# Kernel tuning notes

Measured on AMD Instinct MI355X. Metric: run time of the kernel, lower is better.

The kernel has to match this reference:

```python
import jax, jax.numpy as jnp
import numpy as np

LN_EPS = 1e-5


def setup_inputs() -> dict:
    key = jax.random.key(0)
    ks = jax.random.split(key, 6)
    N_NODES, N_EDGES, D, H, E = 100000, 20000, 128, 64, 1000000
    node_feat = jax.random.normal(ks[0], (N_NODES, D), dtype=jnp.float32)
    edge_feat = jax.random.normal(ks[1], (N_EDGES, D), dtype=jnp.float32)
    gamma = jnp.ones((2 * D,), dtype=jnp.float32)
    beta = jnp.zeros((2 * D,), dtype=jnp.float32)
    # xavier_uniform-like init
    lim1 = float(np.sqrt(6.0 / (2 * D + H)))
    lim2 = float(np.sqrt(6.0 / (H + 1)))
    W1 = jax.random.uniform(ks[2], (2 * D, H), minval=-lim1, maxval=lim1, dtype=jnp.float32)
    b1 = jnp.zeros((H,), dtype=jnp.float32)
    W2 = jax.random.uniform(ks[3], (H, 1), minval=-lim2, maxval=lim2, dtype=jnp.float32)
    b2 = jnp.zeros((1,), dtype=jnp.float32)
    node_idx = jax.random.randint(ks[4], (E,), 0, N_NODES, dtype=jnp.int64 if jax.config.read('jax_enable_x64') else jnp.int32)
    edge_idx = jax.random.randint(ks[5], (E,), 0, N_EDGES, dtype=node_idx.dtype)
    return {"node_feat": node_feat, "edge_feat": edge_feat, "gamma": gamma, "beta": beta,
            "W1": W1, "b1": b1, "W2": W2, "b2": b2,
            "node_idx": node_idx, "edge_idx": edge_idx}


def reference(node_feat, edge_feat, gamma, beta, W1, b1, W2, b2, node_idx, edge_idx):
    # Gather incidence-pair embeddings: [E, D] each
    emb_node = node_feat[node_idx]
    emb_edge = edge_feat[edge_idx]
    # combined: [E, 2D], order = [edge, node] as in torch.cat([emb_edge, emb_node], 1)
    combined = jnp.concatenate([emb_edge, emb_node], axis=1)
    # LayerNorm over last dim
    mu = jnp.mean(combined, axis=-1, keepdims=True)
    var = jnp.var(combined, axis=-1, keepdims=True)
    xn = (combined - mu) * jax.lax.rsqrt(var + LN_EPS) * gamma + beta
    # MLP: Linear -> ReLU -> Linear, output [E, 1]
    h = jax.nn.relu(xn @ W1 + b1)
    return h @ W2 + b2
```

## Files before the change

kernel.cpp:

```cpp
#include <hip/hip_runtime.h>

#define LN_EPS 1e-5f
#define DD 128
#define TWO_D 256
#define HH 64

typedef unsigned int uint;
typedef __attribute__((ext_vector_type(8))) short short8v;
typedef __attribute__((ext_vector_type(4))) float f32x4;

__device__ __forceinline__ unsigned short f2bf(float f) {
    uint u = __float_as_uint(f);
    u += 0x7FFFu + ((u >> 16) & 1u);
    return (unsigned short)(u >> 16);
}
__device__ __forceinline__ float bf2f(unsigned short h) {
    return __uint_as_float(((uint)h) << 16);
}

__global__ __launch_bounds__(256) void k_fused(
    const float* __restrict__ node_feat, int n_nodes, int nbN,
    const float* __restrict__ edge_feat, int n_edges,
    const float* __restrict__ gamma, const float* __restrict__ beta,
    const float* __restrict__ W1, const float* __restrict__ b1,
    signed char* __restrict__ node_pt, float4* __restrict__ node_st,
    signed char* __restrict__ edge_pt, float4* __restrict__ edge_st,
    float* __restrict__ GB) {
    int bid = blockIdx.x;
    int tid = threadIdx.x;

    if (bid == 0) {
        if (tid < 128) {
            int h = tid & 63;
            bool isB = tid >= 64;
            float acc = isB ? b1[h] : 0.f;
            const float* coef = isB ? beta : gamma;
#pragma unroll 8
            for (int d = 0; d < TWO_D; ++d)
                acc = fmaf(coef[d], W1[d * HH + h], acc);
            GB[tid] = acc;
        }
        return;
    }

    const float* feat;
    int nrows, gofs, rbase0;
    signed char* pt;
    float4* st;
    if (bid <= nbN) {
        feat = node_feat; nrows = n_nodes; gofs = 128;
        rbase0 = (bid - 1) * 128; pt = node_pt; st = node_st;
    } else {
        feat = edge_feat; nrows = n_edges; gofs = 0;
        rbase0 = (bid - 1 - nbN) * 128; pt = edge_pt; st = edge_st;
    }

    __shared__ __align__(16) char lds[49664];
    float* scaleLDS = (float*)(lds + 49152);

    {
        int l = tid & 63;
        int w = tid >> 6;
#pragma unroll
        for (int ci = 0; ci < 4; ++ci) {
            int combo = ci * 4 + w;
            int ks = combo & 3;
            int ht = combo >> 2;
            int kbase = gofs + ks * 32 + (l >> 4) * 8;
            int h = ht * 16 + (l & 15);
            short8v v;
#pragma unroll
            for (int j = 0; j < 8; ++j)
                v[j] = (short)f2bf(gamma[kbase + j] * W1[(size_t)(kbase + j) * HH + h]);
            *(short8v*)(lds + 32768 + combo * 1024 + l * 16) = v;
        }
    }

    {
        float4 tmp[16];
#pragma unroll
        for (int u = 0; u < 16; ++u) {
            int F4 = u * 256 + tid;
            int r = F4 >> 5;
            int rg = rbase0 + r;
            rg = rg < nrows ? rg : (nrows - 1);
            int c4 = (F4 & 31) * 4;
            tmp[u] = *(const float4*)&feat[(size_t)rg * DD + c4];
        }
#pragma unroll
        for (int u = 0; u < 16; ++u) {
            int F4 = u * 256 + tid;
            int r = F4 >> 5;
            int c4 = (F4 & 31) * 4;
            uint2 wv;
            wv.x = (uint)f2bf(tmp[u].x) | ((uint)f2bf(tmp[u].y) << 16);
            wv.y = (uint)f2bf(tmp[u].z) | ((uint)f2bf(tmp[u].w) << 16);
            int byte = (r * 256 + c4 * 2) ^ ((r & 7) << 4);
            *(uint2*)(lds + byte) = wv;
        }
    }

    __syncthreads();

    int w = tid >> 6;
    int lane = tid & 63;
    f32x4 acc[2][4];
#pragma unroll
    for (int i = 0; i < 2; ++i)
#pragma unroll
        for (int j = 0; j < 4; ++j) acc[i][j] = (f32x4){0.f, 0.f, 0.f, 0.f};

    int arow_lo = lane & 15;
    int akofs = (lane >> 4) * 8;
#pragma unroll
    for (int ks = 0; ks < 4; ++ks) {
        int kk = ks * 32 + akofs;
        int rr0 = (2 * w) * 16 + arow_lo;
        int rr1 = rr0 + 16;
        short8v a0 = *(const short8v*)(lds + ((rr0 * 256 + kk * 2) ^ ((rr0 & 7) << 4)));
        short8v a1 = *(const short8v*)(lds + ((rr1 * 256 + kk * 2) ^ ((rr1 & 7) << 4)));
#pragma unroll
        for (int ht = 0; ht < 4; ++ht) {
            short8v b = *(const short8v*)(lds + 32768 + (ht * 4 + ks) * 1024 + lane * 16);
            acc[0][ht] = __builtin_amdgcn_mfma_f32_16x16x32_bf16(a0, b, acc[0][ht], 0, 0, 0);
            acc[1][ht] = __builtin_amdgcn_mfma_f32_16x16x32_bf16(a1, b, acc[1][ht], 0, 0, 0);
        }
    }

    {
        int colh = lane & 15;
        int rquad = lane >> 4;
#pragma unroll
        for (int rt = 0; rt < 2; ++rt)
#pragma unroll
            for (int reg = 0; reg < 4; ++reg) {
                float m = fmaxf(fmaxf(fabsf(acc[rt][0][reg]), fabsf(acc[rt][1][reg])),
                                fmaxf(fabsf(acc[rt][2][reg]), fabsf(acc[rt][3][reg])));
                m = fmaxf(m, __shfl_xor(m, 1));
                m = fmaxf(m, __shfl_xor(m, 2));
                m = fmaxf(m, __shfl_xor(m, 4));
                m = fmaxf(m, __shfl_xor(m, 8));
                m = fmaxf(m, 1e-20f);
                float inv = 127.0f / m;
                uint pk = 0;
#pragma unroll
                for (int ht = 0; ht < 4; ++ht) {
                    int q = __float2int_rn(acc[rt][ht][reg] * inv);
                    pk |= ((uint)q & 0xFFu) << (8 * ht);
                }
                int rl = (2 * w + rt) * 16 + rquad * 4 + reg;
                if (rbase0 + rl < nrows)
                    *(uint*)&pt[(size_t)(rbase0 + rl) * 64 + colh * 4] = pk;
                if (colh == 0) scaleLDS[rl] = m * (1.0f / 127.0f);
            }
    }

    __syncthreads();

    {
        int row = tid >> 1, half = tid & 1;
        float s = 0.f, q = 0.f;
#pragma unroll
        for (int i = 0; i < 8; ++i) {
            int byte = (row * 256 + half * 128 + i * 16) ^ ((row & 7) << 4);
            short8v v = *(const short8v*)(lds + byte);
#pragma unroll
            for (int j = 0; j < 8; ++j) {
                float x = bf2f((unsigned short)v[j]);
                s += x;
                q = fmaf(x, x, q);
            }
        }
        s += __shfl_xor(s, 1);
        q += __shfl_xor(q, 1);
        if (half == 0 && rbase0 + row < nrows)
            st[rbase0 + row] = make_float4(s, q, scaleLDS[row], 0.f);
    }
}

__global__ __launch_bounds__(256) void k_pairs(const int* __restrict__ node_idx,
                                               const int* __restrict__ edge_idx,
                                               const signed char* __restrict__ node_pt,
                                               const signed char* __restrict__ edge_pt,
                                               const float4* __restrict__ node_st,
                                               const float4* __restrict__ edge_st,
                                               const float* __restrict__ Gv,
                                               const float* __restrict__ Bv,
                                               const float* __restrict__ W2,
                                               const float* __restrict__ b2,
                                               float* __restrict__ out, int E) {
    int gtid = blockIdx.x * 256 + threadIdx.x;
    int l = gtid & 7;
    int grp = gtid >> 3;
    int ngrps = (gridDim.x * 256) >> 3;

    float G8[8], B8[8], W8[8];
#pragma unroll
    for (int j = 0; j < 8; ++j) {
        int k = l * 8 + j;
        int h = (k & 3) * 16 + (k >> 2);
        G8[j] = Gv[h];
        B8[j] = Bv[h];
        W8[j] = W2[h];
    }
    float b2v = b2[0];

#pragma unroll 4
    for (int p = grp; p < E; p += ngrps) {
        int ni = node_idx[p];
        int ei = edge_idx[p];
        uint2 qe2 = *(const uint2*)&edge_pt[(size_t)ei * 64 + l * 8];
        uint2 qn2 = *(const uint2*)&node_pt[(size_t)ni * 64 + l * 8];
        float4 se = edge_st[ei];
        float4 sn = node_st[ni];

        float S = se.x + sn.x;
        float Q = se.y + sn.y;
        float mu = S * (1.f / TWO_D);
        float var = fmaf(Q, 1.f / TWO_D, -mu * mu);
        float rstd = rsqrtf(var + LN_EPS);
        float nmu = -mu;
        float esc = se.z, nsc = sn.z;

        float acc = 0.f;
#pragma unroll
        for (int j = 0; j < 8; ++j) {
            uint we = (j < 4) ? qe2.x : qe2.y;
            uint wn = (j < 4) ? qn2.x : qn2.y;
            int qa = (int)(signed char)(we >> (8 * (j & 3)));
            int qb = (int)(signed char)(wn >> (8 * (j & 3)));
            float v = fmaf((float)qa, esc, (float)qb * nsc);
            float t = fmaf(nmu, G8[j], v);
            float hv = fmaf(rstd, t, B8[j]);
            hv = fmaxf(hv, 0.f);
            acc = fmaf(hv, W8[j], acc);
        }

        acc += __shfl_xor(acc, 1);
        acc += __shfl_xor(acc, 2);
        acc += __shfl_xor(acc, 4);

        if (l == 0) out[p] = acc + b2v;
    }
}

extern "C" void kernel_launch(void* const* d_in, const int* in_sizes, int n_in,
                              void* d_out, int out_size, void* d_ws, size_t ws_size,
                              hipStream_t stream) {
    const float* node_feat = (const float*)d_in[0];
    const float* edge_feat = (const float*)d_in[1];
    const float* gamma = (const float*)d_in[2];
    const float* beta = (const float*)d_in[3];
    const float* W1 = (const float*)d_in[4];
    const float* b1 = (const float*)d_in[5];
    const float* W2 = (const float*)d_in[6];
    const float* b2 = (const float*)d_in[7];
    const int* node_idx = (const int*)d_in[8];
    const int* edge_idx = (const int*)d_in[9];

    int n_nodes = in_sizes[0] / DD;
    int n_edges = in_sizes[1] / DD;
    int E = in_sizes[8];

    char* wsb = (char*)d_ws;
    size_t o = 0;
    float* GB = (float*)(wsb + o); o += 512;
    float4* node_st = (float4*)(wsb + o); o += (size_t)n_nodes * 16;
    float4* edge_st = (float4*)(wsb + o); o += (size_t)n_edges * 16;
    o = (o + 127) & ~(size_t)127;
    signed char* node_pt = (signed char*)(wsb + o); o += (size_t)n_nodes * 64;
    signed char* edge_pt = (signed char*)(wsb + o); o += (size_t)n_edges * 64;

    int nbN = (n_nodes + 127) / 128;
    int nbE = (n_edges + 127) / 128;

    k_fused<<<1 + nbN + nbE, 256, 0, stream>>>(node_feat, n_nodes, nbN,
                                               edge_feat, n_edges,
                                               gamma, beta, W1, b1,
                                               node_pt, node_st,
                                               edge_pt, edge_st, GB);
    k_pairs<<<2048, 256, 0, stream>>>(node_idx, edge_idx, node_pt, edge_pt,
                                      node_st, edge_st, GB, GB + 64, W2, b2,
                                      (float*)d_out, E);
}
```

Baseline: 54.36 us.

## Shrink per-row stats to 8 bytes and stage indices in LDS per block

Per-row stats change from a float4 (sum, sumsq, scale, pad) to a uint2: sum stays fp32, while sumsq and the quantization scale are packed as bf16. This halves the random-gather traffic for stats in the pair kernel. The pair kernel also drops the grid-stride loop and uses one block per 512 pairs, staging node/edge indices in shared memory with coalesced loads. Storing sumsq in bf16 loses precision in the variance (E[x^2]-mu^2 cancellation), which can introduce error.

```diff
diff --git a/kernel.cpp b/kernel.cpp
--- a/kernel.cpp
+++ b/kernel.cpp
@@ -4,17 +4,19 @@
 #define DD 128
 #define TWO_D 256
 #define HH 64
+#define PPB 512
 
 typedef unsigned int uint;
+typedef unsigned short ushort;
 typedef __attribute__((ext_vector_type(8))) short short8v;
 typedef __attribute__((ext_vector_type(4))) float f32x4;
 
-__device__ __forceinline__ unsigned short f2bf(float f) {
+__device__ __forceinline__ ushort f2bf(float f) {
     uint u = __float_as_uint(f);
     u += 0x7FFFu + ((u >> 16) & 1u);
-    return (unsigned short)(u >> 16);
-}
-__device__ __forceinline__ float bf2f(unsigned short h) {
+    return (ushort)(u >> 16);
+}
+__device__ __forceinline__ float bf2f(ushort h) {
     return __uint_as_float(((uint)h) << 16);
 }
 
@@ -23,8 +25,8 @@
     const float* __restrict__ edge_feat, int n_edges,
     const float* __restrict__ gamma, const float* __restrict__ beta,
     const float* __restrict__ W1, const float* __restrict__ b1,
-    signed char* __restrict__ node_pt, float4* __restrict__ node_st,
-    signed char* __restrict__ edge_pt, float4* __restrict__ edge_st,
+    signed char* __restrict__ node_pt, uint2* __restrict__ node_st,
+    signed char* __restrict__ edge_pt, uint2* __restrict__ edge_st,
     float* __restrict__ GB) {
     int bid = blockIdx.x;
     int tid = threadIdx.x;
@@ -46,7 +48,7 @@
     const float* feat;
     int nrows, gofs, rbase0;
     signed char* pt;
-    float4* st;
+    uint2* st;
     if (bid <= nbN) {
         feat = node_feat; nrows = n_nodes; gofs = 128;
         rbase0 = (bid - 1) * 128; pt = node_pt; st = node_st;
@@ -166,15 +168,17 @@
             short8v v = *(const short8v*)(lds + byte);
 #pragma unroll
             for (int j = 0; j < 8; ++j) {
-                float x = bf2f((unsigned short)v[j]);
+                float x = bf2f((ushort)v[j]);
                 s += x;
                 q = fmaf(x, x, q);
             }
         }
         s += __shfl_xor(s, 1);
         q += __shfl_xor(q, 1);
-        if (half == 0 && rbase0 + row < nrows)
-            st[rbase0 + row] = make_float4(s, q, scaleLDS[row], 0.f);
+        if (half == 0 && rbase0 + row < nrows) {
+            uint packed = ((uint)f2bf(q) << 16) | (uint)f2bf(scaleLDS[row]);
+            st[rbase0 + row] = make_uint2(__float_as_uint(s), packed);
+        }
     }
 }
 
@@ -182,17 +186,27 @@
                                                const int* __restrict__ edge_idx,
                                                const signed char* __restrict__ node_pt,
                                                const signed char* __restrict__ edge_pt,
-                                               const float4* __restrict__ node_st,
-                                               const float4* __restrict__ edge_st,
+                                               const uint2* __restrict__ node_st,
+                                               const uint2* __restrict__ edge_st,
                                                const float* __restrict__ Gv,
                                                const float* __restrict__ Bv,
                                                const float* __restrict__ W2,
                                                const float* __restrict__ b2,
                                                float* __restrict__ out, int E) {
-    int gtid = blockIdx.x * 256 + threadIdx.x;
-    int l = gtid & 7;
-    int grp = gtid >> 3;
-    int ngrps = (gridDim.x * 256) >> 3;
+    __shared__ int sNi[PPB];
+    __shared__ int sEi[PPB];
+    int tid = threadIdx.x;
+    int base = blockIdx.x * PPB;
+    int cnt = E - base;
+    cnt = cnt < PPB ? cnt : PPB;
+    for (int i = tid; i < cnt; i += 256) {
+        sNi[i] = node_idx[base + i];
+        sEi[i] = edge_idx[base + i];
+    }
+    __syncthreads();
+
+    int l = tid & 7;
+    int grp = tid >> 3;
 
     float G8[8], B8[8], W8[8];
 #pragma unroll
@@ -206,27 +220,31 @@
     float b2v = b2[0];
 
 #pragma unroll 4
-    for (int p = grp; p < E; p += ngrps) {
-        int ni = node_idx[p];
-        int ei = edge_idx[p];
+    for (int i = grp; i < cnt; i += 32) {
+        int ni = sNi[i];
+        int ei = sEi[i];
         uint2 qe2 = *(const uint2*)&edge_pt[(size_t)ei * 64 + l * 8];
         uint2 qn2 = *(const uint2*)&node_pt[(size_t)ni * 64 + l * 8];
-        float4 se = edge_st[ei];
-        float4 sn = node_st[ni];
-
-        float S = se.x + sn.x;
-        float Q = se.y + sn.y;
+        uint2 se = edge_st[ei];
+        uint2 sn = node_st[ni];
+
+        float S = __uint_as_float(se.x) + __uint_as_float(sn.x);
+        float Q = bf2f((ushort)(se.y >> 16)) + bf2f((ushort)(sn.y >> 16));
+        float esc = bf2f((ushort)(se.y & 0xFFFFu));
+        float nsc = bf2f((ushort)(sn.y & 0xFFFFu));
+
         float mu = S * (1.f / TWO_D);
         float var = fmaf(Q, 1.f / TWO_D, -mu * mu);
         float rstd = rsqrtf(var + LN_EPS);
         float nmu = -mu;
-        float esc = se.z, nsc = sn.z;
-
+
+        uint ue_[4] = {qe2.x, qe2.y, 0, 0};
+        uint un_[4] = {qn2.x, qn2.y, 0, 0};
         float acc = 0.f;
 #pragma unroll
         for (int j = 0; j < 8; ++j) {
-            uint we = (j < 4) ? qe2.x : qe2.y;
-            uint wn = (j < 4) ? qn2.x : qn2.y;
+            uint we = (j < 4) ? ue_[0] : ue_[1];
+            uint wn = (j < 4) ? un_[0] : un_[1];
             int qa = (int)(signed char)(we >> (8 * (j & 3)));
             int qb = (int)(signed char)(wn >> (8 * (j & 3)));
             float v = fmaf((float)qa, esc, (float)qb * nsc);
@@ -240,7 +258,7 @@
         acc += __shfl_xor(acc, 2);
         acc += __shfl_xor(acc, 4);
 
-        if (l == 0) out[p] = acc + b2v;
+        if (l == 0) out[base + i] = acc + b2v;
     }
 }
 
@@ -265,8 +283,8 @@
     char* wsb = (char*)d_ws;
     size_t o = 0;
     float* GB = (float*)(wsb + o); o += 512;
-    float4* node_st = (float4*)(wsb + o); o += (size_t)n_nodes * 16;
-    float4* edge_st = (float4*)(wsb + o); o += (size_t)n_edges * 16;
+    uint2* node_st = (uint2*)(wsb + o); o += (size_t)n_nodes * 8;
+    uint2* edge_st = (uint2*)(wsb + o); o += (size_t)n_edges * 8;
     o = (o + 127) & ~(size_t)127;
     signed char* node_pt = (signed char*)(wsb + o); o += (size_t)n_nodes * 64;
     signed char* edge_pt = (signed char*)(wsb + o); o += (size_t)n_edges * 64;
@@ -279,7 +297,7 @@
                                                gamma, beta, W1, b1,
                                                node_pt, node_st,
                                                edge_pt, edge_st, GB);
-    k_pairs<<<2048, 256, 0, stream>>>(node_idx, edge_idx, node_pt, edge_pt,
-                                      node_st, edge_st, GB, GB + 64, W2, b2,
-                                      (float*)d_out, E);
-}
+    k_pairs<<<(E + PPB - 1) / PPB, 256, 0, stream>>>(node_idx, edge_idx, node_pt, edge_pt,
+                                                     node_st, edge_st, GB, GB + 64, W2, b2,
+                                                     (float*)d_out, E);
+}
```

Result: faster. 52.41 us (-3.6%).
